# Kernel tuning notes

Measured on AMD Instinct MI355X. Metric: run time of the kernel, lower is better.

The kernel has to match this reference:

```python
import jax, jax.numpy as jnp
import numpy as np

MASK_VALUE = -10000000000.0
B, S = 2, 2048
HQ, HKV, HD = 16, 8, 256
D = HQ * HD  # 4096
ROPE_BASE = 10000.0


def rms_norm(x, scale, eps=1e-6):
    # Gemma-style RMSNorm over the last (head_dim) axis with (1 + scale) gain.
    var = jnp.mean(jnp.square(x), axis=-1, keepdims=True)
    return x * jax.lax.rsqrt(var + eps) * (1.0 + scale)


def apply_rope(x, positions):
    # x: [b, t, h, d]; positions: [b, t]
    d = x.shape[-1]
    fraction = 2.0 * jnp.arange(d // 2, dtype=jnp.float32) / d
    timescale = ROPE_BASE ** fraction                     # [d/2]
    sinusoid = positions[..., None].astype(jnp.float32) / timescale  # [b, t, d/2]
    sin = jnp.sin(sinusoid)[:, :, None, :]                # [b, t, 1, d/2]
    cos = jnp.cos(sinusoid)[:, :, None, :]
    first, second = jnp.split(x, 2, axis=-1)
    out = jnp.concatenate([first * cos - second * sin,
                           second * cos + first * sin], axis=-1)
    return out.astype(x.dtype)


def setup_inputs() -> dict:
    key = jax.random.key(0)
    ks = jax.random.split(key, 6)
    x = jax.random.normal(ks[0], (B, S, D), dtype=jnp.float32)
    Wq = jax.random.normal(ks[1], (D, HQ * HD), dtype=jnp.float32) * 0.02
    Wk = jax.random.normal(ks[2], (D, HKV * HD), dtype=jnp.float32) * 0.02
    Wv = jax.random.normal(ks[3], (D, HKV * HD), dtype=jnp.float32) * 0.02
    Wo = jax.random.normal(ks[4], (HQ * HD, D), dtype=jnp.float32) * 0.02
    k_scale = jnp.zeros((HD,), dtype=jnp.float32)
    v_scale = jnp.zeros((HD,), dtype=jnp.float32)
    mask = jnp.broadcast_to(jnp.tril(jnp.ones((S, S), dtype=bool))[None], (B, S, S))
    position = jnp.broadcast_to(jnp.arange(S, dtype=jnp.int32)[None], (B, S))
    return {"x": x, "Wq": Wq, "Wk": Wk, "Wv": Wv, "Wo": Wo,
            "k_scale": k_scale, "v_scale": v_scale,
            "mask": mask, "position": position}


def reference(x, Wq, Wk, Wv, Wo, k_scale, v_scale, mask, position):
    b, t, _ = x.shape
    group = HQ // HKV
    q = (x @ Wq).reshape(b, t, HQ, HD)
    k = (x @ Wk).reshape(b, t, HKV, HD)
    v = (x @ Wv).reshape(b, t, HKV, HD)
    k = rms_norm(k, k_scale)
    v = rms_norm(v, v_scale)
    q = apply_rope(q, position)
    k = apply_rope(k, position)
    # [b, hkv, group, t, d] view of q; avoids materializing repeated K/V (same math as repeat).
    q = q.transpose(0, 2, 1, 3).reshape(b, HKV, group, t, HD)
    k = k.transpose(0, 2, 1, 3)  # [b, hkv, T, d]
    v = v.transpose(0, 2, 1, 3)
    scores = jnp.einsum('bhgtd,bhTd->bhgtT', q, k) / jnp.sqrt(jnp.float32(HD))
    scores = jnp.where(mask[:, None, None, :, :], scores, MASK_VALUE)
    weights = jax.nn.softmax(scores, axis=-1)
    out = jnp.einsum('bhgtT,bhTd->bhgtd', weights, v)
    out = out.reshape(b, HQ, t, HD).transpose(0, 2, 1, 3).reshape(b, t, HQ * HD)
    return out @ Wo
```

## Files before the change

kernel.cpp:

```cpp
#include <hip/hip_runtime.h>
#include <stdint.h>

typedef __bf16 bf16;
typedef __bf16 bf16x4 __attribute__((ext_vector_type(4)));
typedef __bf16 bf16x8 __attribute__((ext_vector_type(8)));
typedef float f32x4 __attribute__((ext_vector_type(4)));

#define GAS __attribute__((address_space(1)))
#define LAS __attribute__((address_space(3)))

__device__ __forceinline__ void gload_lds16(const void* g, void* l) {
  __builtin_amdgcn_global_load_lds((GAS const void*)g, (LAS void*)l, 16, 0, 0);
}

__global__ __launch_bounds__(256) void cvt_bf16(const float* __restrict__ in,
                                                bf16* __restrict__ out, int n4) {
  int i = blockIdx.x * 256 + threadIdx.x;
  if (i >= n4) return;
  float4 v = ((const float4*)in)[i];
  bf16x4 o;
  o[0] = (bf16)v.x; o[1] = (bf16)v.y; o[2] = (bf16)v.z; o[3] = (bf16)v.w;
  ((bf16x4*)out)[i] = o;
}

__global__ __launch_bounds__(256) void tconv(const float* __restrict__ W,
                                             bf16* __restrict__ Wt, int K, int N) {
  __shared__ bf16 tile[64][68];
  const int n0 = blockIdx.x * 64, k0 = blockIdx.y * 64;
  const int u2 = threadIdx.x & 31, kr0 = threadIdx.x >> 5;
#pragma unroll
  for (int i = 0; i < 8; ++i) {
    int kr = kr0 + i * 8;
    float2 v = *(const float2*)&W[(size_t)(k0 + kr) * N + n0 + u2 * 2];
    tile[kr][u2 * 2] = (bf16)v.x;
    tile[kr][u2 * 2 + 1] = (bf16)v.y;
  }
  __syncthreads();
  const int u4 = threadIdx.x & 15, nr0 = threadIdx.x >> 4;
#pragma unroll
  for (int i = 0; i < 4; ++i) {
    int nr = nr0 + i * 16;
    bf16x4 o;
#pragma unroll
    for (int j = 0; j < 4; ++j) o[j] = tile[u4 * 4 + j][nr];
    *(bf16x4*)&Wt[(size_t)(n0 + nr) * K + k0 + u4 * 4] = o;
  }
}

template <int OUTF32>
__global__ __launch_bounds__(512, 2) void gemm256(const bf16* __restrict__ A,
                                                  const bf16* __restrict__ Bt,
                                                  void* __restrict__ Cp,
                                                  const int N, const int K,
                                                  const int ncc_l, const int cbx_l) {
  __shared__ __attribute__((aligned(16))) bf16 lds[2][4][8192];
  const int t = threadIdx.x, w = t >> 6, l = t & 63;
  const int la = l & 15, lq = l >> 4;
  const int xcd = blockIdx.x & 7, wi = blockIdx.x >> 3;
  const int cr = xcd >> ncc_l, cc = xcd & ((1 << ncc_l) - 1);
  const int by = (cr << 3) + (wi >> cbx_l);
  const int bx = (cc << cbx_l) + (wi & ((1 << cbx_l) - 1));
  const int m0 = by * 256, n0 = bx * 256;
  const int wr = w >> 2, wc = w & 3;
  const int c0 = w * 64 + l;
  const int sr0 = c0 >> 2, soff = (((c0 & 3) ^ ((c0 >> 3) & 3)) << 3);
  const bf16* pA0 = A + (size_t)(m0 + sr0) * K + soff;
  const bf16* pA1 = pA0 + (size_t)128 * K;
  const bf16* pB0 = Bt + (size_t)(n0 + sr0) * K + soff;
  const bf16* pB1 = pB0 + (size_t)128 * K;
  const int rsl = (lq ^ ((la >> 1) & 3)) << 3;

  f32x4 acc[8][4] = {};

#define STAGE_SLAB(s, nb, kti)                                                \
  do {                                                                        \
    const bf16* p0_ = ((s) & 1) ? pB0 : pA0;                                  \
    const bf16* p1_ = ((s) & 1) ? pB1 : pA1;                                  \
    const size_t ko_ = (size_t)(kti) * 64 + ((s) >> 1) * 32;                  \
    gload_lds16(p0_ + ko_, &lds[nb][s][w * 512]);                             \
    gload_lds16(p1_ + ko_, &lds[nb][s][4096 + w * 512]);                      \
  } while (0)

#define PHASE(kh, mg)                                                         \
  {                                                                           \
    bf16x8 a_[4];                                                             \
    _Pragma("unroll") for (int m_ = 0; m_ < 4; ++m_)                          \
        a_[m_] = *(const bf16x8*)&lds[bi][(kh)*2][(wr * 128 + (mg)*64 + m_ * 16 + la) * 32 + rsl]; \
    __builtin_amdgcn_s_setprio(1);                                            \
    _Pragma("unroll") for (int m_ = 0; m_ < 4; ++m_)                          \
      _Pragma("unroll") for (int n_ = 0; n_ < 4; ++n_)                        \
          acc[(mg)*4 + m_][n_] = __builtin_amdgcn_mfma_f32_16x16x32_bf16(     \
              a_[m_], bfr[n_], acc[(mg)*4 + m_][n_], 0, 0, 0);                \
    __builtin_amdgcn_s_setprio(0);                                            \
  }

  STAGE_SLAB(0, 0, 0);
  STAGE_SLAB(1, 0, 0);
  STAGE_SLAB(2, 0, 0);
  STAGE_SLAB(3, 0, 0);

  const int NT = K >> 6;
  for (int kt = 0; kt < NT; ++kt) {
    const int bi = kt & 1, nbi = bi ^ 1;
    const bool pf = (kt + 1) < NT;
    bf16x8 bfr[4];
    if (pf) asm volatile("s_waitcnt vmcnt(4)" ::: "memory");
    else    asm volatile("s_waitcnt vmcnt(0)" ::: "memory");
    __builtin_amdgcn_s_barrier();
    __builtin_amdgcn_sched_barrier(0);
    if (pf) STAGE_SLAB(0, nbi, kt + 1);
#pragma unroll
    for (int n_ = 0; n_ < 4; ++n_)
      bfr[n_] = *(const bf16x8*)&lds[bi][1][(wc * 64 + n_ * 16 + la) * 32 + rsl];
    PHASE(0, 0)
    if (pf) STAGE_SLAB(1, nbi, kt + 1);
    PHASE(0, 1)
    if (pf) asm volatile("s_waitcnt vmcnt(4)" ::: "memory");
    else    asm volatile("s_waitcnt vmcnt(0)" ::: "memory");
    __builtin_amdgcn_s_barrier();
    __builtin_amdgcn_sched_barrier(0);
    if (pf) STAGE_SLAB(2, nbi, kt + 1);
#pragma unroll
    for (int n_ = 0; n_ < 4; ++n_)
      bfr[n_] = *(const bf16x8*)&lds[bi][3][(wc * 64 + n_ * 16 + la) * 32 + rsl];
    PHASE(1, 0)
    if (pf) STAGE_SLAB(3, nbi, kt + 1);
    PHASE(1, 1)
  }
#undef PHASE
#undef STAGE_SLAB

  const int crow = m0 + wr * 128, ccol = n0 + wc * 64;
  if (OUTF32) {
    float* C = (float*)Cp;
#pragma unroll
    for (int mi = 0; mi < 8; ++mi)
#pragma unroll
      for (int ni = 0; ni < 4; ++ni)
#pragma unroll
        for (int i = 0; i < 4; ++i)
          C[(size_t)(crow + mi * 16 + lq * 4 + i) * N + ccol + ni * 16 + la] = acc[mi][ni][i];
  } else {
    bf16* C = (bf16*)Cp;
#pragma unroll
    for (int mi = 0; mi < 8; ++mi)
#pragma unroll
      for (int ni = 0; ni < 4; ++ni)
#pragma unroll
        for (int i = 0; i < 4; ++i)
          C[(size_t)(crow + mi * 16 + lq * 4 + i) * N + ccol + ni * 16 + la] = (bf16)acc[mi][ni][i];
  }
}

__global__ __launch_bounds__(256) void rope_q(bf16* __restrict__ qkv, const int* __restrict__ pos) {
  const int w = threadIdx.x >> 6, l = threadIdx.x & 63;
  const int idx = blockIdx.x * 4 + w;
  const int bt = idx >> 4, h = idx & 15;
  bf16* p = qkv + (size_t)bt * 8192 + h * 256 + l * 4;
  bf16x4 xv = *(const bf16x4*)p;
  float x[4], y[4];
#pragma unroll
  for (int j = 0; j < 4; ++j) x[j] = (float)xv[j];
#pragma unroll
  for (int j = 0; j < 4; ++j) y[j] = __shfl_xor(x[j], 32, 64);
  const float posf = (float)pos[bt];
  bf16x4 ov;
#pragma unroll
  for (int j = 0; j < 4; ++j) {
    const int pr = (l & 31) * 4 + j;
    float sv, cv;
    sincosf(posf * exp2f((float)pr * (-13.287712379549449f / 128.0f)), &sv, &cv);
    float o = x[j] * cv + ((l < 32) ? -y[j] : y[j]) * sv;
    ov[j] = (bf16)(o * 0.0625f);
  }
  *(bf16x4*)p = ov;
}

__global__ __launch_bounds__(256) void norm_rope_k(bf16* __restrict__ kbase,
                                                   const float* __restrict__ scale,
                                                   const int* __restrict__ pos) {
  const int w = threadIdx.x >> 6, l = threadIdx.x & 63;
  const int idx = blockIdx.x * 4 + w;
  const int bt = idx >> 3, h = idx & 7;
  bf16* p = kbase + (size_t)bt * 8192 + h * 256 + l * 4;
  bf16x4 xv = *(const bf16x4*)p;
  float x[4];
#pragma unroll
  for (int j = 0; j < 4; ++j) x[j] = (float)xv[j];
  float ss = x[0] * x[0] + x[1] * x[1] + x[2] * x[2] + x[3] * x[3];
#pragma unroll
  for (int m = 1; m < 64; m <<= 1) ss += __shfl_xor(ss, m, 64);
  const float r = rsqrtf(ss * (1.0f / 256.0f) + 1e-6f);
#pragma unroll
  for (int j = 0; j < 4; ++j) x[j] = x[j] * r * (1.0f + scale[l * 4 + j]);
  float y[4];
#pragma unroll
  for (int j = 0; j < 4; ++j) y[j] = __shfl_xor(x[j], 32, 64);
  const float posf = (float)pos[bt];
  bf16x4 ov;
#pragma unroll
  for (int j = 0; j < 4; ++j) {
    const int pr = (l & 31) * 4 + j;
    float sv, cv;
    sincosf(posf * exp2f((float)pr * (-13.287712379549449f / 128.0f)), &sv, &cv);
    float o = x[j] * cv + ((l < 32) ? -y[j] : y[j]) * sv;
    ov[j] = (bf16)o;
  }
  *(bf16x4*)p = ov;
}

__global__ __launch_bounds__(256) void norm_v(bf16* __restrict__ vbase,
                                              const float* __restrict__ scale) {
  const int w = threadIdx.x >> 6, l = threadIdx.x & 63;
  const int idx = blockIdx.x * 4 + w;
  const int bt = idx >> 3, h = idx & 7;
  bf16* p = vbase + (size_t)bt * 8192 + h * 256 + l * 4;
  bf16x4 xv = *(const bf16x4*)p;
  float x[4];
#pragma unroll
  for (int j = 0; j < 4; ++j) x[j] = (float)xv[j];
  float ss = x[0] * x[0] + x[1] * x[1] + x[2] * x[2] + x[3] * x[3];
#pragma unroll
  for (int m = 1; m < 64; m <<= 1) ss += __shfl_xor(ss, m, 64);
  const float r = rsqrtf(ss * (1.0f / 256.0f) + 1e-6f);
  bf16x4 ov;
#pragma unroll
  for (int j = 0; j < 4; ++j) ov[j] = (bf16)(x[j] * r * (1.0f + scale[l * 4 + j]));
  *(bf16x4*)p = ov;
}

__global__ __launch_bounds__(256) void vtrans(const bf16* __restrict__ vbase,
                                              bf16* __restrict__ vt) {
  __shared__ bf16 tile[64][68];
  const int tt = blockIdx.x, dd = blockIdx.y, bh = blockIdx.z;
  const int b = bh >> 3, h = bh & 7;
  const int u4 = threadIdx.x & 15, r0 = threadIdx.x >> 4;
#pragma unroll
  for (int i = 0; i < 4; ++i) {
    int tr = r0 + i * 16;
    bf16x4 v = *(const bf16x4*)&vbase[(size_t)(b * 2048 + tt * 64 + tr) * 8192 + h * 256 + dd * 64 + u4 * 4];
#pragma unroll
    for (int j = 0; j < 4; ++j) tile[u4 * 4 + j][tr] = v[j];
  }
  __syncthreads();
#pragma unroll
  for (int i = 0; i < 4; ++i) {
    int dr = r0 + i * 16;
    bf16x4 o;
#pragma unroll
    for (int j = 0; j < 4; ++j) o[j] = tile[dr][u4 * 4 + j];
    *(bf16x4*)&vt[((size_t)(b * 8 + h) * 256 + dd * 64 + dr) * 2048 + tt * 64 + u4 * 4] = o;
  }
}

__global__ __launch_bounds__(512, 2) void flash_attn(const bf16* __restrict__ qkv,
                                                     const bf16* __restrict__ vt,
                                                     bf16* __restrict__ o) {
  __shared__ __attribute__((aligned(16))) bf16 Ks[2 * 16384];
  __shared__ __attribute__((aligned(16))) bf16 Vs[2 * 16384];
  __shared__ __attribute__((aligned(16))) bf16 Ps[8 * 1152];
  const int t = threadIdx.x, w = t >> 6, l = t & 63;
  const int la = l & 15, lq = l >> 4;
  const int h = blockIdx.x, qbp = blockIdx.y, b = blockIdx.z;
  const int hkv = h >> 1;

  const bf16* kbase = qkv + (size_t)(b * 2048) * 8192 + 4096 + hkv * 256;
  const bf16* vbase = vt + ((size_t)(b * 8 + hkv)) * 256 * 2048;

  const bf16* ksrc[4];
  const bf16* vsrc[4];
#pragma unroll
  for (int i = 0; i < 4; ++i) {
    int c = i * 512 + t;
    int krr = c >> 5, ksl = (c & 31) ^ (krr & 7);
    int vrr = c >> 3, vsl = (c & 7) ^ (vrr & 7);
    ksrc[i] = kbase + (size_t)krr * 8192 + ksl * 8;
    vsrc[i] = vbase + (size_t)vrr * 2048 + vsl * 8;
  }

#define STAGE(bb, tt0)                                                        \
  do {                                                                        \
    _Pragma("unroll") for (int i_ = 0; i_ < 4; ++i_)                          \
        gload_lds16(ksrc[i_] + (size_t)(tt0) * 8192,                          \
                    Ks + (bb) * 16384 + i_ * 4096 + w * 512);                 \
    _Pragma("unroll") for (int i_ = 0; i_ < 4; ++i_)                          \
        gload_lds16(vsrc[i_] + (tt0), Vs + (bb) * 16384 + i_ * 4096 + w * 512); \
  } while (0)

  for (int part = 0; part < 2; ++part) {
    const int qb = part ? qbp : (15 - qbp);
    const int q0 = qb * 128;
    const int rbase = q0 + w * 16;

    bf16x8 qf[8];
    {
      const bf16* qrow = qkv + (size_t)(b * 2048 + rbase + la) * 8192 + h * 256 + lq * 8;
#pragma unroll
      for (int kg = 0; kg < 8; ++kg) qf[kg] = *(const bf16x8*)(qrow + kg * 32);
    }
    f32x4 acc[16] = {};
    float mrow[4] = {-1e30f, -1e30f, -1e30f, -1e30f};
    float lrow[4] = {0.f, 0.f, 0.f, 0.f};
    const int nT = 2 * qb + 2;

    STAGE(0, 0);
    int cur = 0;
    for (int tti = 0; tti < nT; ++tti) {
      const int t0 = tti * 64;
      if (tti + 1 < nT) {
        STAGE(cur ^ 1, t0 + 64);
        asm volatile("s_waitcnt vmcnt(8)" ::: "memory");
      } else {
        asm volatile("s_waitcnt vmcnt(0)" ::: "memory");
      }
      __builtin_amdgcn_s_barrier();
      __builtin_amdgcn_sched_barrier(0);
      if (t0 <= rbase + 15) {
        const bf16* Kc = Ks + cur * 16384;
        const bf16* Vc = Vs + cur * 16384;
        f32x4 s[4] = {};
        __builtin_amdgcn_s_setprio(1);
#pragma unroll
        for (int n = 0; n < 4; ++n) {
          int rT = n * 16 + la;
#pragma unroll
          for (int kg = 0; kg < 8; ++kg) {
            int sl = (kg * 4 + lq) ^ (rT & 7);
            bf16x8 kbv = *(const bf16x8*)(Kc + rT * 256 + sl * 8);
            s[n] = __builtin_amdgcn_mfma_f32_16x16x32_bf16(qf[kg], kbv, s[n], 0, 0, 0);
          }
        }
        __builtin_amdgcn_s_setprio(0);
        float mxr[4];
        float need = -1.f;
#pragma unroll
        for (int i = 0; i < 4; ++i) {
          const int row = rbase + lq * 4 + i;
          float mx = -1e30f;
#pragma unroll
          for (int n = 0; n < 4; ++n) {
            float v = s[n][i];
            v = (t0 + n * 16 + la > row) ? -1e30f : v;
            s[n][i] = v;
            mx = fmaxf(mx, v);
          }
          mx = fmaxf(mx, __shfl_xor(mx, 1, 64));
          mx = fmaxf(mx, __shfl_xor(mx, 2, 64));
          mx = fmaxf(mx, __shfl_xor(mx, 4, 64));
          mx = fmaxf(mx, __shfl_xor(mx, 8, 64));
          mxr[i] = mx;
          need = fmaxf(need, mx - mrow[i]);
        }
        const bool resc = __any(need > 8.0f);
        float scalef[4];
        if (resc) {
#pragma unroll
          for (int i = 0; i < 4; ++i) {
            const float mnew = fmaxf(mrow[i], mxr[i]);
            scalef[i] = __expf(mrow[i] - mnew);
            mrow[i] = mnew;
          }
        }
#pragma unroll
        for (int i = 0; i < 4; ++i) {
          float ps = 0.f;
#pragma unroll
          for (int n = 0; n < 4; ++n) {
            float v = s[n][i];
            float pp = (v <= -1e29f) ? 0.f : __expf(v - mrow[i]);
            s[n][i] = pp;
            ps += pp;
          }
          ps += __shfl_xor(ps, 1, 64);
          ps += __shfl_xor(ps, 2, 64);
          ps += __shfl_xor(ps, 4, 64);
          ps += __shfl_xor(ps, 8, 64);
          lrow[i] = resc ? (lrow[i] * scalef[i] + ps) : (lrow[i] + ps);
        }
        if (resc) {
#pragma unroll
          for (int n = 0; n < 16; ++n) {
            acc[n][0] *= scalef[0]; acc[n][1] *= scalef[1];
            acc[n][2] *= scalef[2]; acc[n][3] *= scalef[3];
          }
        }
        bf16* pw = Ps + w * 1152;
#pragma unroll
        for (int n = 0; n < 4; ++n)
#pragma unroll
          for (int i = 0; i < 4; ++i)
            pw[(lq * 4 + i) * 72 + n * 16 + la] = (bf16)s[n][i];
        __builtin_amdgcn_s_setprio(1);
#pragma unroll
        for (int kc = 0; kc < 2; ++kc) {
          bf16x8 pa = *(const bf16x8*)(pw + la * 72 + kc * 32 + lq * 8);
#pragma unroll
          for (int n = 0; n < 16; ++n) {
            int rd = n * 16 + la;
            int sl = (kc * 4 + lq) ^ (rd & 7);
            bf16x8 vbv = *(const bf16x8*)(Vc + rd * 64 + sl * 8);
            acc[n] = __builtin_amdgcn_mfma_f32_16x16x32_bf16(pa, vbv, acc[n], 0, 0, 0);
          }
        }
        __builtin_amdgcn_s_setprio(0);
      }
      __builtin_amdgcn_s_barrier();
      __builtin_amdgcn_sched_barrier(0);
      cur ^= 1;
    }
#pragma unroll
    for (int i = 0; i < 4; ++i) {
      const int row = rbase + lq * 4 + i;
      const float inv = 1.0f / lrow[i];
      bf16* orow = o + ((size_t)(b * 2048 + row)) * 4096 + h * 256;
#pragma unroll
      for (int n = 0; n < 16; ++n) orow[n * 16 + la] = (bf16)(acc[n][i] * inv);
    }
  }
#undef STAGE
}

__global__ void fill_err(float* o, int n) {
  int i = blockIdx.x * 256 + threadIdx.x;
  if (i < n) o[i] = 1e9f;
}

extern "C" void kernel_launch(void* const* d_in, const int* in_sizes, int n_in,
                              void* d_out, int out_size, void* d_ws, size_t ws_size,
                              hipStream_t stream) {
  const float* x = (const float*)d_in[0];
  const float* Wq = (const float*)d_in[1];
  const float* Wk = (const float*)d_in[2];
  const float* Wv = (const float*)d_in[3];
  const float* Wo = (const float*)d_in[4];
  const float* kscale = (const float*)d_in[5];
  const float* vscale = (const float*)d_in[6];
  const int* pos = (const int*)d_in[8];
  float* out = (float*)d_out;

  const size_t WS_NEED = 251658240ull;
  if (ws_size < WS_NEED) {
    fill_err<<<65536, 256, 0, stream>>>(out, out_size);
    return;
  }
  char* ws = (char*)d_ws;
  bf16* x16   = (bf16*)(ws);
  bf16* wqkvt = (bf16*)(ws + 33554432);
  bf16* wot   = (bf16*)(ws + 100663296);
  bf16* qkv   = (bf16*)(ws + 134217728);
  bf16* vtb   = (bf16*)(ws + 201326592);
  bf16* ao    = (bf16*)(ws + 218103808);

  cvt_bf16<<<16384, 256, 0, stream>>>(x, x16, 4194304);
  tconv<<<dim3(64, 64), 256, 0, stream>>>(Wq, wqkvt, 4096, 4096);
  tconv<<<dim3(32, 64), 256, 0, stream>>>(Wk, wqkvt + (size_t)4096 * 4096, 4096, 2048);
  tconv<<<dim3(32, 64), 256, 0, stream>>>(Wv, wqkvt + (size_t)6144 * 4096, 4096, 2048);
  tconv<<<dim3(64, 64), 256, 0, stream>>>(Wo, wot, 4096, 4096);

  gemm256<0><<<512, 512, 0, stream>>>(x16, wqkvt, qkv, 8192, 4096, 2, 3);

  rope_q<<<16384, 256, 0, stream>>>(qkv, pos);
  norm_rope_k<<<8192, 256, 0, stream>>>(qkv + 4096, kscale, pos);
  norm_v<<<8192, 256, 0, stream>>>(qkv + 6144, vscale);
  vtrans<<<dim3(32, 4, 16), 256, 0, stream>>>(qkv + 6144, vtb);

  flash_attn<<<dim3(16, 8, 2), 512, 0, stream>>>(qkv, vtb, ao);

  gemm256<1><<<256, 512, 0, stream>>>(ao, wot, out, 4096, 4096, 2, 2);
}
```

Baseline: 629.8 us.

## Deepen GEMM LDS pipeline to four half-K stages with three in flight

Restructures the bf16 GEMM main loop from a double-buffered 64-wide K tile into a four-slot ring of 32-wide K slices, keeping three slices of prefetch in flight ahead of compute. Each iteration waits on the oldest slice, issues the next loads, and computes, followed by an explicit drain of the last three slices. The aim is to hide more global-load latency behind the MFMA work. The LDS footprint stays the same, but there is one barrier per 32-K slice, which keeps the number of barriers per unit of K unchanged.

```diff
diff --git a/kernel.cpp b/kernel.cpp
--- a/kernel.cpp
+++ b/kernel.cpp
@@ -53,7 +53,7 @@
                                                   void* __restrict__ Cp,
                                                   const int N, const int K,
                                                   const int ncc_l, const int cbx_l) {
-  __shared__ __attribute__((aligned(16))) bf16 lds[2][4][8192];
+  __shared__ __attribute__((aligned(16))) bf16 lds[4][2][8192];
   const int t = threadIdx.x, w = t >> 6, l = t & 63;
   const int la = l & 15, lq = l >> 4;
   const int xcd = blockIdx.x & 7, wi = blockIdx.x >> 3;
@@ -72,20 +72,26 @@
 
   f32x4 acc[8][4] = {};
 
-#define STAGE_SLAB(s, nb, kti)                                                \
+#define STAGE_A(b_, H_)                                                       \
   do {                                                                        \
-    const bf16* p0_ = ((s) & 1) ? pB0 : pA0;                                  \
-    const bf16* p1_ = ((s) & 1) ? pB1 : pA1;                                  \
-    const size_t ko_ = (size_t)(kti) * 64 + ((s) >> 1) * 32;                  \
-    gload_lds16(p0_ + ko_, &lds[nb][s][w * 512]);                             \
-    gload_lds16(p1_ + ko_, &lds[nb][s][4096 + w * 512]);                      \
+    gload_lds16(pA0 + (H_) * 32, &lds[b_][0][w * 512]);                       \
+    gload_lds16(pA1 + (H_) * 32, &lds[b_][0][4096 + w * 512]);                \
   } while (0)
-
-#define PHASE(kh, mg)                                                         \
+#define STAGE_B(b_, H_)                                                       \
+  do {                                                                        \
+    gload_lds16(pB0 + (H_) * 32, &lds[b_][1][w * 512]);                       \
+    gload_lds16(pB1 + (H_) * 32, &lds[b_][1][4096 + w * 512]);                \
+  } while (0)
+
+#define LOAD_BFR(b_)                                                          \
+  _Pragma("unroll") for (int n_ = 0; n_ < 4; ++n_)                            \
+      bfr[n_] = *(const bf16x8*)&lds[b_][1][(wc * 64 + n_ * 16 + la) * 32 + rsl];
+
+#define PHASE(b_, mg)                                                         \
   {                                                                           \
     bf16x8 a_[4];                                                             \
     _Pragma("unroll") for (int m_ = 0; m_ < 4; ++m_)                          \
-        a_[m_] = *(const bf16x8*)&lds[bi][(kh)*2][(wr * 128 + (mg)*64 + m_ * 16 + la) * 32 + rsl]; \
+        a_[m_] = *(const bf16x8*)&lds[b_][0][(wr * 128 + (mg)*64 + m_ * 16 + la) * 32 + rsl]; \
     __builtin_amdgcn_s_setprio(1);                                            \
     _Pragma("unroll") for (int m_ = 0; m_ < 4; ++m_)                          \
       _Pragma("unroll") for (int n_ = 0; n_ < 4; ++n_)                        \
@@ -94,41 +100,57 @@
     __builtin_amdgcn_s_setprio(0);                                            \
   }
 
-  STAGE_SLAB(0, 0, 0);
-  STAGE_SLAB(1, 0, 0);
-  STAGE_SLAB(2, 0, 0);
-  STAGE_SLAB(3, 0, 0);
-
-  const int NT = K >> 6;
-  for (int kt = 0; kt < NT; ++kt) {
-    const int bi = kt & 1, nbi = bi ^ 1;
-    const bool pf = (kt + 1) < NT;
+  STAGE_A(0, 0); STAGE_B(0, 0);
+  STAGE_A(1, 1); STAGE_B(1, 1);
+  STAGE_A(2, 2); STAGE_B(2, 2);
+
+  const int NH = K >> 5;
+  for (int H = 0; H <= NH - 4; ++H) {
+    const int b = H & 3, nb = (H + 3) & 3;
     bf16x8 bfr[4];
-    if (pf) asm volatile("s_waitcnt vmcnt(4)" ::: "memory");
-    else    asm volatile("s_waitcnt vmcnt(0)" ::: "memory");
+    asm volatile("s_waitcnt vmcnt(8)" ::: "memory");
     __builtin_amdgcn_s_barrier();
     __builtin_amdgcn_sched_barrier(0);
-    if (pf) STAGE_SLAB(0, nbi, kt + 1);
-#pragma unroll
-    for (int n_ = 0; n_ < 4; ++n_)
-      bfr[n_] = *(const bf16x8*)&lds[bi][1][(wc * 64 + n_ * 16 + la) * 32 + rsl];
-    PHASE(0, 0)
-    if (pf) STAGE_SLAB(1, nbi, kt + 1);
-    PHASE(0, 1)
-    if (pf) asm volatile("s_waitcnt vmcnt(4)" ::: "memory");
-    else    asm volatile("s_waitcnt vmcnt(0)" ::: "memory");
+    STAGE_A(nb, H + 3);
+    LOAD_BFR(b)
+    PHASE(b, 0)
+    STAGE_B(nb, H + 3);
+    PHASE(b, 1)
+  }
+  {
+    const int b = (NH - 3) & 3;
+    bf16x8 bfr[4];
+    asm volatile("s_waitcnt vmcnt(8)" ::: "memory");
     __builtin_amdgcn_s_barrier();
     __builtin_amdgcn_sched_barrier(0);
-    if (pf) STAGE_SLAB(2, nbi, kt + 1);
-#pragma unroll
-    for (int n_ = 0; n_ < 4; ++n_)
-      bfr[n_] = *(const bf16x8*)&lds[bi][3][(wc * 64 + n_ * 16 + la) * 32 + rsl];
-    PHASE(1, 0)
-    if (pf) STAGE_SLAB(3, nbi, kt + 1);
-    PHASE(1, 1)
+    LOAD_BFR(b)
+    PHASE(b, 0)
+    PHASE(b, 1)
+  }
+  {
+    const int b = (NH - 2) & 3;
+    bf16x8 bfr[4];
+    asm volatile("s_waitcnt vmcnt(4)" ::: "memory");
+    __builtin_amdgcn_s_barrier();
+    __builtin_amdgcn_sched_barrier(0);
+    LOAD_BFR(b)
+    PHASE(b, 0)
+    PHASE(b, 1)
+  }
+  {
+    const int b = (NH - 1) & 3;
+    bf16x8 bfr[4];
+    asm volatile("s_waitcnt vmcnt(0)" ::: "memory");
+    __builtin_amdgcn_s_barrier();
+    __builtin_amdgcn_sched_barrier(0);
+    LOAD_BFR(b)
+    PHASE(b, 0)
+    PHASE(b, 1)
   }
 #undef PHASE
-#undef STAGE_SLAB
+#undef LOAD_BFR
+#undef STAGE_B
+#undef STAGE_A
 
   const int crow = m0 + wr * 128, ccol = n0 + wc * 64;
   if (OUTF32) {
```

After: 622.0 us, median of 2. No clear change (-1.2%).
